# Kernel optimization log

Measured on AMD Instinct MI355X. Metric: run time of the kernel, lower is better.

The kernel has to match this reference:

```python
import jax, jax.numpy as jnp
import numpy as np


def setup_inputs() -> dict:
    key = jax.random.key(0)
    k1, k2, k3 = jax.random.split(key, 3)
    B, S, H, E = 8, 4096, 1024, 8
    x = jax.random.normal(k1, (B, S, H), dtype=jnp.float32)
    W_router = jax.random.normal(k2, (H, E), dtype=jnp.float32) * (1.0 / np.sqrt(H))
    b_router = jnp.zeros((E,), dtype=jnp.float32)
    W_expert = jax.random.normal(k3, (H, H), dtype=jnp.float32) * (1.0 / np.sqrt(H))
    b_expert = jnp.zeros((H,), dtype=jnp.float32)
    return {"x": x, "W_router": W_router, "b_router": b_router,
            "W_expert": W_expert, "b_expert": b_expert}


def reference(x, W_router, b_router, W_expert, b_expert):
    B, S, H = x.shape
    h = x.reshape(-1, H)                       # [T, H], T = B*S
    logits = h @ W_router + b_router           # [T, E]
    probs = jax.nn.softmax(logits, axis=1)     # normalized_logits
    best = jnp.argmax(probs, axis=1)           # index_of_best_expert [T]
    order = jnp.argsort(best)                  # optimal_index (token permutation)
    sorted_h = h[order]                        # gather: sorted_hidden_states
    # single-process all-to-all is identity; single expert FFN on permuted tokens
    expert_out = sorted_h @ W_expert + b_expert  # [T, H]
    # faithful to source: output is NOT unpermuted before reshape
    out = expert_out.reshape(B, S, H)
    best_p = jnp.take_along_axis(probs, best[:, None], axis=1)[:, 0]  # [T]
    return out * best_p.reshape(B, S, 1)
```

## Files before the change

kernel.cpp:

```cpp
#include <hip/hip_runtime.h>
#include <hip/hip_bf16.h>
#include <math.h>

#define T_TOK 32768
#define HD 1024
#define NE 8

typedef _Float16 half8 __attribute__((ext_vector_type(8)));
typedef _Float16 half4v __attribute__((ext_vector_type(4)));
typedef float f32x4 __attribute__((ext_vector_type(4)));

__device__ __forceinline__ void gload16(const void* g, void* l) {
  __builtin_amdgcn_global_load_lds((const __attribute__((address_space(1))) void*)g,
                                   (__attribute__((address_space(3))) void*)l,
                                   16, 0, 0);
}

__global__ __launch_bounds__(256) void router_k(const float* __restrict__ x,
                                                const float* __restrict__ Wr,
                                                const float* __restrict__ br,
                                                int* __restrict__ best,
                                                float* __restrict__ bestp) {
  const int lane = threadIdx.x & 63;
  const int w = threadIdx.x >> 6;
  const int t = blockIdx.x * 4 + w;
  const float4* h4 = (const float4*)(x + (size_t)t * HD);
  const float4* wr4 = (const float4*)Wr;
  double p[NE];
#pragma unroll
  for (int e = 0; e < NE; ++e) p[e] = 0.0;
#pragma unroll
  for (int i = 0; i < 4; ++i) {
    const int k4 = lane + 64 * i;
    float4 v = h4[k4];
    float vv[4] = {v.x, v.y, v.z, v.w};
#pragma unroll
    for (int u = 0; u < 4; ++u) {
      const int k = k4 * 4 + u;
      float4 w0 = wr4[k * 2];
      float4 w1 = wr4[k * 2 + 1];
      double hv = (double)vv[u];
      p[0] += hv * (double)w0.x; p[1] += hv * (double)w0.y;
      p[2] += hv * (double)w0.z; p[3] += hv * (double)w0.w;
      p[4] += hv * (double)w1.x; p[5] += hv * (double)w1.y;
      p[6] += hv * (double)w1.z; p[7] += hv * (double)w1.w;
    }
  }
#pragma unroll
  for (int off = 32; off > 0; off >>= 1) {
#pragma unroll
    for (int e = 0; e < NE; ++e) p[e] += __shfl_xor(p[e], off);
  }
#pragma unroll
  for (int e = 0; e < NE; ++e) p[e] += (double)br[e];
  int be = 0; double bm = p[0];
#pragma unroll
  for (int e = 1; e < NE; ++e) if (p[e] > bm) { bm = p[e]; be = e; }
  double s = 0.0;
#pragma unroll
  for (int e = 0; e < NE; ++e) s += exp(p[e] - bm);
  if (lane == 0) { best[t] = be; bestp[t] = (float)(1.0 / s); }
}

__global__ __launch_bounds__(1024) void sort_k(const int* __restrict__ best,
                                               int* __restrict__ order) {
  __shared__ int s[1024][NE];
  const int i = threadIdx.x;
  int c[NE];
#pragma unroll
  for (int e = 0; e < NE; ++e) c[e] = 0;
  const int t0 = i * 32;
  for (int j = 0; j < 32; ++j) c[best[t0 + j]]++;
#pragma unroll
  for (int e = 0; e < NE; ++e) s[i][e] = c[e];
  __syncthreads();
  for (int d = 1; d < 1024; d <<= 1) {
    int v[NE];
    if (i >= d) {
#pragma unroll
      for (int e = 0; e < NE; ++e) v[e] = s[i - d][e];
    }
    __syncthreads();
    if (i >= d) {
#pragma unroll
      for (int e = 0; e < NE; ++e) s[i][e] += v[e];
    }
    __syncthreads();
  }
  int basee[NE]; int a = 0;
#pragma unroll
  for (int e = 0; e < NE; ++e) { basee[e] = a; a += s[1023][e]; }
  int pos[NE];
#pragma unroll
  for (int e = 0; e < NE; ++e) pos[e] = basee[e] + s[i][e] - c[e];
  for (int j = 0; j < 32; ++j) {
    int t = t0 + j;
    int e = best[t];
    order[pos[e]++] = t;
  }
}

__global__ __launch_bounds__(256) void wtrans_k(const float* __restrict__ W,
                                                _Float16* __restrict__ Wt) {
  __shared__ float tile[32][33];
  const int tx = threadIdx.x & 31, ty = threadIdx.x >> 5;
  const int kb = blockIdx.x * 32, nb = blockIdx.y * 32;
#pragma unroll
  for (int i = 0; i < 4; ++i)
    tile[ty + 8 * i][tx] = W[(size_t)(kb + ty + 8 * i) * HD + nb + tx];
  __syncthreads();
#pragma unroll
  for (int i = 0; i < 4; ++i)
    Wt[(size_t)(nb + ty + 8 * i) * HD + kb + tx] = (_Float16)tile[tx][ty + 8 * i];
}

__global__ __launch_bounds__(256) void gather_k(const float* __restrict__ x,
                                                const int* __restrict__ order,
                                                _Float16* __restrict__ A16) {
  const int row = blockIdx.x;
  const int src = order[row];
  const float4* in = (const float4*)(x + (size_t)src * HD);
  float4 v = in[threadIdx.x];
  half4v o = { (_Float16)v.x, (_Float16)v.y, (_Float16)v.z, (_Float16)v.w };
  ((half4v*)(A16 + (size_t)row * HD))[threadIdx.x] = o;
}

#define BM 128
#define BN 128
#define BK 32

__global__ __launch_bounds__(256) void gemm_k(const _Float16* __restrict__ A,
                                              const _Float16* __restrict__ Bt,
                                              const float* __restrict__ bias,
                                              const float* __restrict__ scale,
                                              float* __restrict__ out) {
  __shared__ alignas(16) _Float16 As[BM * BK];
  __shared__ alignas(16) _Float16 Bs[BN * BK];
  const int tid = threadIdx.x;
  const int w = tid >> 6, lane = tid & 63;
  const int wm = w >> 1, wn = w & 1;
  const int u = lane >> 4, r16 = lane & 15;
  const int mb = blockIdx.y, nb = blockIdx.x;
  const size_t abase = (size_t)mb * BM * HD;
  const size_t bbase = (size_t)nb * BN * HD;
  f32x4 acc[4][4];
#pragma unroll
  for (int m = 0; m < 4; ++m)
#pragma unroll
    for (int n = 0; n < 4; ++n) acc[m][n] = (f32x4){0.f, 0.f, 0.f, 0.f};

  for (int kt = 0; kt < HD / BK; ++kt) {
    __syncthreads();
#pragma unroll
    for (int i = 0; i < 2; ++i) {
      const int chunk = i * 4 + w;
      const int li = chunk * 64 + lane;
      const int row = li >> 2, col = li & 3;
      gload16(A + abase + (size_t)row * HD + kt * BK + col * 8, As + chunk * 512);
      gload16(Bt + bbase + (size_t)row * HD + kt * BK + col * 8, Bs + chunk * 512);
    }
    __syncthreads();
    half8 af[4], bf[4];
#pragma unroll
    for (int m = 0; m < 4; ++m)
      af[m] = *(const half8*)(As + (wm * 64 + m * 16 + r16) * BK + u * 8);
#pragma unroll
    for (int n = 0; n < 4; ++n)
      bf[n] = *(const half8*)(Bs + (wn * 64 + n * 16 + r16) * BK + u * 8);
#pragma unroll
    for (int m = 0; m < 4; ++m)
#pragma unroll
      for (int n = 0; n < 4; ++n)
        acc[m][n] = __builtin_amdgcn_mfma_f32_16x16x32_f16(af[m], bf[n], acc[m][n], 0, 0, 0);
  }
  const int colg0 = nb * BN + wn * 64 + r16;
  const int rowg0 = mb * BM + wm * 64 + u * 4;
  float bl[4];
#pragma unroll
  for (int n = 0; n < 4; ++n) bl[n] = bias[colg0 + n * 16];
#pragma unroll
  for (int m = 0; m < 4; ++m) {
#pragma unroll
    for (int j = 0; j < 4; ++j) {
      const int rowg = rowg0 + m * 16 + j;
      const float sc = scale[rowg];
      float* op = out + (size_t)rowg * HD;
#pragma unroll
      for (int n = 0; n < 4; ++n)
        op[colg0 + n * 16] = (acc[m][n][j] + bl[n]) * sc;
    }
  }
}

extern "C" void kernel_launch(void* const* d_in, const int* in_sizes, int n_in,
                              void* d_out, int out_size, void* d_ws, size_t ws_size,
                              hipStream_t stream) {
  const float* x  = (const float*)d_in[0];
  const float* Wr = (const float*)d_in[1];
  const float* br = (const float*)d_in[2];
  const float* We = (const float*)d_in[3];
  const float* be = (const float*)d_in[4];
  float* out = (float*)d_out;

  char* wsb = (char*)d_ws;
  int*      best  = (int*)wsb;
  float*    bestp = (float*)(wsb + 131072);
  int*      order = (int*)(wsb + 262144);
  _Float16* Wt16  = (_Float16*)(wsb + 393216);
  _Float16* A16   = (_Float16*)(wsb + 393216 + 2097152);

  hipLaunchKernelGGL(wtrans_k, dim3(32, 32), dim3(256), 0, stream, We, Wt16);
  hipLaunchKernelGGL(router_k, dim3(T_TOK / 4), dim3(256), 0, stream, x, Wr, br, best, bestp);
  hipLaunchKernelGGL(sort_k, dim3(1), dim3(1024), 0, stream, best, order);
  hipLaunchKernelGGL(gather_k, dim3(T_TOK), dim3(256), 0, stream, x, order, A16);
  hipLaunchKernelGGL(gemm_k, dim3(HD / BN, T_TOK / BM), dim3(256), 0, stream,
                     A16, Wt16, be, bestp, out);
}
```

Baseline: 466.5 us.

## Parallelize expert sort into hist/scan/scatter and cut router reduction shuffles

New measurement: 452.9 us. -2.9%, faster.

```diff
diff --git a/kernel.cpp b/kernel.cpp
--- a/kernel.cpp
+++ b/kernel.cpp
@@ -26,17 +26,16 @@
   const int t = blockIdx.x * 4 + w;
   const float4* h4 = (const float4*)(x + (size_t)t * HD);
   const float4* wr4 = (const float4*)Wr;
-  double p[NE];
-#pragma unroll
-  for (int e = 0; e < NE; ++e) p[e] = 0.0;
+  float4 xv[4];
+#pragma unroll
+  for (int i = 0; i < 4; ++i) xv[i] = h4[lane + 64 * i];
+  double p[NE] = {0, 0, 0, 0, 0, 0, 0, 0};
 #pragma unroll
   for (int i = 0; i < 4; ++i) {
-    const int k4 = lane + 64 * i;
-    float4 v = h4[k4];
-    float vv[4] = {v.x, v.y, v.z, v.w};
+    float vv[4] = {xv[i].x, xv[i].y, xv[i].z, xv[i].w};
 #pragma unroll
     for (int u = 0; u < 4; ++u) {
-      const int k = k4 * 4 + u;
+      const int k = (lane + 64 * i) * 4 + u;
       float4 w0 = wr4[k * 2];
       float4 w1 = wr4[k * 2 + 1];
       double hv = (double)vv[u];
@@ -47,57 +46,86 @@
     }
   }
 #pragma unroll
-  for (int off = 32; off > 0; off >>= 1) {
-#pragma unroll
-    for (int e = 0; e < NE; ++e) p[e] += __shfl_xor(p[e], off);
-  }
-#pragma unroll
-  for (int e = 0; e < NE; ++e) p[e] += (double)br[e];
-  int be = 0; double bm = p[0];
-#pragma unroll
-  for (int e = 1; e < NE; ++e) if (p[e] > bm) { bm = p[e]; be = e; }
-  double s = 0.0;
-#pragma unroll
-  for (int e = 0; e < NE; ++e) s += exp(p[e] - bm);
-  if (lane == 0) { best[t] = be; bestp[t] = (float)(1.0 / s); }
-}
-
-__global__ __launch_bounds__(1024) void sort_k(const int* __restrict__ best,
-                                               int* __restrict__ order) {
-  __shared__ int s[1024][NE];
-  const int i = threadIdx.x;
-  int c[NE];
-#pragma unroll
-  for (int e = 0; e < NE; ++e) c[e] = 0;
-  const int t0 = i * 32;
-  for (int j = 0; j < 32; ++j) c[best[t0 + j]]++;
-#pragma unroll
-  for (int e = 0; e < NE; ++e) s[i][e] = c[e];
-  __syncthreads();
-  for (int d = 1; d < 1024; d <<= 1) {
-    int v[NE];
-    if (i >= d) {
-#pragma unroll
-      for (int e = 0; e < NE; ++e) v[e] = s[i - d][e];
-    }
-    __syncthreads();
-    if (i >= d) {
-#pragma unroll
-      for (int e = 0; e < NE; ++e) s[i][e] += v[e];
-    }
-    __syncthreads();
-  }
-  int basee[NE]; int a = 0;
-#pragma unroll
-  for (int e = 0; e < NE; ++e) { basee[e] = a; a += s[1023][e]; }
-  int pos[NE];
-#pragma unroll
-  for (int e = 0; e < NE; ++e) pos[e] = basee[e] + s[i][e] - c[e];
-  for (int j = 0; j < 32; ++j) {
-    int t = t0 + j;
-    int e = best[t];
-    order[pos[e]++] = t;
-  }
+  for (int d = 1; d <= 4; d <<= 1)
+#pragma unroll
+    for (int e = 0; e < NE; ++e) p[e] += __shfl_xor(p[e], d);
+  const int el = lane & 7;
+  double a0 = (el & 1) ? p[1] : p[0];
+  double a1 = (el & 1) ? p[3] : p[2];
+  double a2 = (el & 1) ? p[5] : p[4];
+  double a3 = (el & 1) ? p[7] : p[6];
+  double b0 = (el & 2) ? a1 : a0;
+  double b1 = (el & 2) ? a3 : a2;
+  double q  = (el & 4) ? b1 : b0;
+#pragma unroll
+  for (int d = 8; d <= 32; d <<= 1) q += __shfl_xor(q, d);
+  q += (double)br[el];
+  double mq = q; int mi = el;
+#pragma unroll
+  for (int d = 1; d <= 4; d <<= 1) {
+    double oq = __shfl_xor(mq, d);
+    int    oi = __shfl_xor(mi, d);
+    if (oq > mq || (oq == mq && oi < mi)) { mq = oq; mi = oi; }
+  }
+  float ex = __expf((float)(q - mq));
+#pragma unroll
+  for (int d = 1; d <= 4; d <<= 1) ex += __shfl_xor(ex, d);
+  if (lane == 0) { best[t] = mi; bestp[t] = 1.0f / ex; }
+}
+
+__global__ __launch_bounds__(256) void hist_k(const int* __restrict__ best,
+                                              int* __restrict__ hist) {
+  __shared__ int h[NE];
+  if (threadIdx.x < NE) h[threadIdx.x] = 0;
+  __syncthreads();
+  const int t = blockIdx.x * 256 + threadIdx.x;
+  atomicAdd(&h[best[t]], 1);
+  __syncthreads();
+  if (threadIdx.x < NE) hist[blockIdx.x * NE + threadIdx.x] = h[threadIdx.x];
+}
+
+__global__ __launch_bounds__(1024) void scan_k(const int* __restrict__ hist,
+                                               int* __restrict__ offs) {
+  __shared__ int s[NE][129];
+  __shared__ int ebase[NE];
+  const int e = threadIdx.x >> 7, b = threadIdx.x & 127;
+  const int v = hist[b * NE + e];
+  s[e][b] = v;
+  __syncthreads();
+  for (int d = 1; d < 128; d <<= 1) {
+    int add = (b >= d) ? s[e][b - d] : 0;
+    __syncthreads();
+    s[e][b] += add;
+    __syncthreads();
+  }
+  if (threadIdx.x == 0) {
+    int a = 0;
+#pragma unroll
+    for (int ee = 0; ee < NE; ++ee) { ebase[ee] = a; a += s[ee][127]; }
+  }
+  __syncthreads();
+  offs[b * NE + e] = ebase[e] + s[e][b] - v;
+}
+
+__global__ __launch_bounds__(256) void scatter_k(const int* __restrict__ best,
+                                                 const int* __restrict__ offs,
+                                                 int* __restrict__ order) {
+  __shared__ int whist[4][NE];
+  const int tid = threadIdx.x, wv = tid >> 6, lane = tid & 63;
+  const int t = blockIdx.x * 256 + tid;
+  const int e = best[t];
+  const unsigned long long lower = (lane == 63) ? ~0ull >> 1 : (1ull << lane) - 1;
+  int myrank = 0;
+#pragma unroll
+  for (int E = 0; E < NE; ++E) {
+    unsigned long long m = __ballot(e == E);
+    if (e == E) myrank = __popcll(m & lower);
+    if (lane == 0) whist[wv][E] = __popcll(m);
+  }
+  __syncthreads();
+  int base = 0;
+  for (int pw = 0; pw < wv; ++pw) base += whist[pw][e];
+  order[offs[blockIdx.x * NE + e] + base + myrank] = t;
 }
 
 __global__ __launch_bounds__(256) void wtrans_k(const float* __restrict__ W,
@@ -206,12 +234,16 @@
   int*      best  = (int*)wsb;
   float*    bestp = (float*)(wsb + 131072);
   int*      order = (int*)(wsb + 262144);
-  _Float16* Wt16  = (_Float16*)(wsb + 393216);
-  _Float16* A16   = (_Float16*)(wsb + 393216 + 2097152);
+  int*      hist  = (int*)(wsb + 393216);
+  int*      offs  = (int*)(wsb + 397312);
+  _Float16* Wt16  = (_Float16*)(wsb + 401408);
+  _Float16* A16   = (_Float16*)(wsb + 401408 + 2097152);
 
   hipLaunchKernelGGL(wtrans_k, dim3(32, 32), dim3(256), 0, stream, We, Wt16);
   hipLaunchKernelGGL(router_k, dim3(T_TOK / 4), dim3(256), 0, stream, x, Wr, br, best, bestp);
-  hipLaunchKernelGGL(sort_k, dim3(1), dim3(1024), 0, stream, best, order);
+  hipLaunchKernelGGL(hist_k, dim3(T_TOK / 256), dim3(256), 0, stream, best, hist);
+  hipLaunchKernelGGL(scan_k, dim3(1), dim3(1024), 0, stream, hist, offs);
+  hipLaunchKernelGGL(scatter_k, dim3(T_TOK / 256), dim3(256), 0, stream, best, offs, order);
   hipLaunchKernelGGL(gather_k, dim3(T_TOK), dim3(256), 0, stream, x, order, A16);
   hipLaunchKernelGGL(gemm_k, dim3(HD / BN, T_TOK / BM), dim3(256), 0, stream,
                      A16, Wt16, be, bestp, out);
```
